# Performance work log

Measured on AMD Instinct MI355X. Metric: run time of the kernel, lower is better.

Reference implementation:

```python
import jax, jax.numpy as jnp
import numpy as np

B, T, D, H = 4, 2048, 1024, 16
Dh = D // H

def setup_inputs() -> dict:
    key = jax.random.key(0)
    ks = jax.random.split(key, 6)
    scale = 1.0 / np.sqrt(D)
    return {
        "x": jax.random.normal(ks[0], (B, T, D), dtype=jnp.float32),
        "W_q": jax.random.normal(ks[1], (D, D), dtype=jnp.float32) * scale,
        "W_k": jax.random.normal(ks[2], (D, D), dtype=jnp.float32) * scale,
        "W_v": jax.random.normal(ks[3], (D, D), dtype=jnp.float32) * scale,
        "W_o": jax.random.normal(ks[4], (D, D), dtype=jnp.float32) * scale,
        "b_o": jax.random.normal(ks[5], (D,), dtype=jnp.float32) * 0.02,
    }

def reference(x, W_q, W_k, W_v, W_o, b_o):
    # Linear weights stored torch-style (out, in): y = x @ W.T
    def split_heads(z):
        return z.reshape(B, T, H, Dh).transpose(0, 2, 1, 3)  # [B,H,T,Dh]
    q = split_heads(x @ W_q.T)
    k = split_heads(x @ W_k.T)
    v = split_heads(x @ W_v.T)
    scale = Dh ** -0.5
    attn = jnp.einsum('bhqd,bhkd->bhqk', q, k) * scale  # [B,H,T,T]
    causal = jnp.tril(jnp.ones((T, T), dtype=bool))
    attn = jnp.where(causal[None, None], attn, -jnp.inf)
    attn = jax.nn.softmax(attn, axis=-1)
    y = jnp.einsum('bhqk,bhkd->bhqd', attn, v)  # [B,H,T,Dh]
    y = y.transpose(0, 2, 1, 3).reshape(B, T, D)
    return y @ W_o.T + b_o
```

## Files before the change

kernel.cpp:

```cpp
#include <hip/hip_runtime.h>
#include <hip/hip_bf16.h>
#include <stdint.h>

#define B_   4
#define T_   2048
#define H_   16
#define MTOT (B_ * T_)
#define NQKV 3072
#define QSC  0.18033688f

typedef __attribute__((ext_vector_type(8))) __bf16 bf16x8;
typedef __attribute__((ext_vector_type(4))) float f32x4;
typedef __attribute__((ext_vector_type(16))) float f32x16;
typedef __attribute__((ext_vector_type(4))) float f4v;
typedef __attribute__((ext_vector_type(4))) unsigned short us4;
typedef __attribute__((ext_vector_type(8))) unsigned short us8;
typedef __attribute__((ext_vector_type(4))) unsigned int u32x4;

static __device__ __forceinline__ unsigned short f2bf(float f) {
  __hip_bfloat16 h = __float2bfloat16(f);
  return __builtin_bit_cast(unsigned short, h);
}

static __device__ __forceinline__ float fast_exp2(float x) {
#if __has_builtin(__builtin_amdgcn_exp2f)
  return __builtin_amdgcn_exp2f(x);
#else
  float r; asm("v_exp_f32 %0, %1" : "=v"(r) : "v"(x)); return r;
#endif
}

static __device__ __forceinline__ void async16(const void* g, void* l) {
  __builtin_amdgcn_global_load_lds(
      (const __attribute__((address_space(1))) void*)g,
      (__attribute__((address_space(3))) void*)l, 16, 0, 0);
}

__global__ __launch_bounds__(256) void cvt_all(
    const float* __restrict__ x, const float* __restrict__ Wq,
    const float* __restrict__ Wk, const float* __restrict__ Wv,
    const float* __restrict__ Wo, unsigned short* __restrict__ xb,
    unsigned short* __restrict__ wqkv, unsigned short* __restrict__ wo) {
  int i = blockIdx.x * blockDim.x + threadIdx.x;
  const float* s; unsigned short* d; int j;
  if (i < 2097152)      { s = x;  d = xb;             j = i; }
  else if (i < 2359296) { s = Wq; d = wqkv;           j = i - 2097152; }
  else if (i < 2621440) { s = Wk; d = wqkv + 1048576; j = i - 2359296; }
  else if (i < 2883584) { s = Wv; d = wqkv + 2097152; j = i - 2621440; }
  else                  { s = Wo; d = wo;             j = i - 2883584; }
  f4v v = reinterpret_cast<const f4v*>(s)[j];
  us4 o;
  o.x = f2bf(v.x); o.y = f2bf(v.y); o.z = f2bf(v.z); o.w = f2bf(v.w);
  reinterpret_cast<us4*>(d)[j] = o;
}

template <int MODE>
__global__ __launch_bounds__(256) void gemm_bt(
    const unsigned short* __restrict__ A,
    const unsigned short* __restrict__ Bw,
    unsigned short* __restrict__ Cb,
    float* __restrict__ Cf,
    const float* __restrict__ bias,
    int K, int N) {
  __shared__ __align__(16) unsigned short As[128 * 32];
  __shared__ __align__(16) unsigned short Bs[128 * 32];

  const int t = threadIdx.x;
  const int lane = t & 63;
  const int w = t >> 6;
  const int lr = lane & 15;
  const int lg = lane >> 4;
  const int wm = w >> 1;
  const int wn = w & 1;
  const int m0 = blockIdx.y * 128;
  const int n0 = blockIdx.x * 128;

  f32x4 acc[4][4];
#pragma unroll
  for (int i = 0; i < 4; ++i)
#pragma unroll
    for (int j = 0; j < 4; ++j) acc[i][j] = (f32x4){0.f, 0.f, 0.f, 0.f};

  const int srow = t >> 2;
  const int scol = (t & 3) * 8;
  const unsigned short* ga = A + (size_t)(m0 + srow) * K + scol;
  const unsigned short* gb = Bw + (size_t)(n0 + srow) * K + scol;

  for (int k0 = 0; k0 < K; k0 += 32) {
    async16(ga + k0,                  &As[t * 8]);
    async16(ga + k0 + (size_t)64 * K, &As[2048 + t * 8]);
    async16(gb + k0,                  &Bs[t * 8]);
    async16(gb + k0 + (size_t)64 * K, &Bs[2048 + t * 8]);
    __syncthreads();

    bf16x8 af[4], bfr[4];
#pragma unroll
    for (int mi = 0; mi < 4; ++mi)
      af[mi] = *(const bf16x8*)&As[(wm * 64 + mi * 16 + lr) * 32 + lg * 8];
#pragma unroll
    for (int ni = 0; ni < 4; ++ni)
      bfr[ni] = *(const bf16x8*)&Bs[(wn * 64 + ni * 16 + lr) * 32 + lg * 8];
#pragma unroll
    for (int mi = 0; mi < 4; ++mi)
#pragma unroll
      for (int ni = 0; ni < 4; ++ni)
        acc[mi][ni] = __builtin_amdgcn_mfma_f32_16x16x32_bf16(
            af[mi], bfr[ni], acc[mi][ni], 0, 0, 0);
    __syncthreads();
  }

#pragma unroll
  for (int mi = 0; mi < 4; ++mi) {
    const int row = m0 + wm * 64 + mi * 16 + lg * 4;
#pragma unroll
    for (int ni = 0; ni < 4; ++ni) {
      const int col = n0 + wn * 64 + ni * 16 + lr;
#pragma unroll
      for (int r = 0; r < 4; ++r) {
        if (MODE == 1) {
          Cf[(size_t)(row + r) * N + col] = acc[mi][ni][r] + bias[col];
        } else {
          float v = acc[mi][ni][r];
          if (col < 1024) v *= QSC;
          Cb[(size_t)(row + r) * N + col] = f2bf(v);
        }
      }
    }
  }
}

__global__ __launch_bounds__(512, 2) void attn_kernel(
    const unsigned short* __restrict__ qkv, unsigned short* __restrict__ ob) {
  const int bid = blockIdx.x;
  const int qg = (bid < 256) ? (7 - (bid >> 6)) : ((bid - 256) >> 6);
  const int pair = bid & 63;
  const int b = pair >> 4;
  const int h = pair & 15;
  const int t = threadIdx.x;
  const int w = t >> 6;
  const int lane = t & 63;
  const int l31 = lane & 31;
  const int hi = lane >> 5;

  const int q0w = qg * 256 + w * 32;
  const int myBound = qg * 4 + (w >> 1);
  const int NT2 = qg * 2 + 2;

  __shared__ __align__(16) unsigned short Ks[2][128 * 64];
  __shared__ __align__(16) unsigned short Vs[2][128 * 64];

  const size_t rowbase = (size_t)(b * T_) * NQKV;

  bf16x8 Qf[4];
  {
    const unsigned short* qp =
        qkv + rowbase + (size_t)(q0w + l31) * NQKV + h * 64 + hi * 8;
#pragma unroll
    for (int m = 0; m < 4; ++m) Qf[m] = *(const bf16x8*)(qp + m * 16);
  }

  const int krow = t >> 3;
  const int kg = (t & 7) ^ (krow & 7);
  const unsigned short* kbase =
      qkv + rowbase + 1024 + h * 64 + kg * 8 + (size_t)krow * NQKV;
  const int kvr = t >> 3;
  const int dc = t & 7;
  const unsigned short* vbase =
      qkv + rowbase + 2048 + h * 64 + dc * 8 + (size_t)kvr * NQKV;

  float m_i = -INFINITY, l_i = 0.f;
  f32x16 o[2];
#pragma unroll
  for (int r = 0; r < 16; ++r) { o[0][r] = 0.f; o[1][r] = 0.f; }

#define VSCATTER(Vb, v0, v1)                                     \
  {                                                              \
    _Pragma("unroll") for (int i = 0; i < 8; ++i) {              \
      const int sw = dc ^ i;                                     \
      const int c0 = (kvr >> 3) ^ sw;                            \
      unsigned short* vp = (Vb) + (dc * 8 + i) * 128 + (kvr & 7);\
      vp[c0 * 8] = (v0)[i];                                      \
      vp[c0 * 8 + 64] = (v1)[i];                                 \
    }                                                            \
  }

  {
    async16(kbase, &Ks[0][t * 8]);
    async16(kbase + (size_t)64 * NQKV, &Ks[0][4096 + t * 8]);
    us8 v0 = *(const us8*)vbase;
    us8 v1 = *(const us8*)(vbase + (size_t)64 * NQKV);
    VSCATTER(&Vs[0][0], v0, v1);
  }

  int cur = 0;
  for (int kt = 0; kt < NT2; ++kt) {
    __syncthreads();

    const bool pf = (kt + 1 < NT2);
    us8 v0, v1;
    if (pf) {
      const size_t off = (size_t)(kt + 1) * 128 * NQKV;
      async16(kbase + off, &Ks[cur ^ 1][t * 8]);
      async16(kbase + off + (size_t)64 * NQKV, &Ks[cur ^ 1][4096 + t * 8]);
      v0 = *(const us8*)(vbase + off);
      v1 = *(const us8*)(vbase + off + (size_t)64 * NQKV);
    }

    const unsigned short* Kb = Ks[cur];
    const unsigned short* Vb = Vs[cur];

#pragma unroll
    for (int kh = 0; kh < 2; ++kh) {
      const int kt64 = kt * 2 + kh;
      if (kt64 > myBound) break;

      f32x16 a0, a1;
#pragma unroll
      for (int r = 0; r < 16; ++r) { a0[r] = 0.f; a1[r] = 0.f; }
      {
        const int rb0 = (kh * 64 + l31) * 64;
        const int rb1 = (kh * 64 + 32 + l31) * 64;
        const int r7 = l31 & 7;
        __builtin_amdgcn_s_setprio(1);
#pragma unroll
        for (int m = 0; m < 4; ++m) {
          const int c = (((m << 1) | hi) ^ r7) * 8;
          bf16x8 kf0 = *(const bf16x8*)&Kb[rb0 + c];
          bf16x8 kf1 = *(const bf16x8*)&Kb[rb1 + c];
          a0 = __builtin_amdgcn_mfma_f32_32x32x16_bf16(kf0, Qf[m], a0, 0, 0, 0);
          a1 = __builtin_amdgcn_mfma_f32_32x32x16_bf16(kf1, Qf[m], a1, 0, 0, 0);
        }
        __builtin_amdgcn_s_setprio(0);
      }

      if (kt64 == myBound) {
        const int qglob = q0w + l31;
#pragma unroll
        for (int r = 0; r < 16; ++r) {
          const int kvb = kt64 * 64 + (r & 3) + ((r >> 2) << 3) + (hi << 2);
          if (kvb > qglob) a0[r] = -INFINITY;
          if (kvb + 32 > qglob) a1[r] = -INFINITY;
        }
      }

      float m8[8];
#pragma unroll
      for (int j = 0; j < 8; ++j)
        m8[j] = fmaxf(fmaxf(a0[j], a0[j + 8]), fmaxf(a1[j], a1[j + 8]));
      float pmax = fmaxf(fmaxf(fmaxf(m8[0], m8[4]), fmaxf(m8[1], m8[5])),
                         fmaxf(fmaxf(m8[2], m8[6]), fmaxf(m8[3], m8[7])));
      pmax = fmaxf(pmax, __shfl_xor(pmax, 32));
      if (__any(pmax > m_i + 8.f)) {
        const float mnew = fmaxf(m_i, pmax);
        const float al = fast_exp2(m_i - mnew);
        m_i = mnew;
        l_i *= al;
#pragma unroll
        for (int r = 0; r < 16; ++r) { o[0][r] *= al; o[1][r] *= al; }
      }

#pragma unroll
      for (int r = 0; r < 16; ++r) {
        a0[r] = fast_exp2(a0[r] - m_i);
        a1[r] = fast_exp2(a1[r] - m_i);
      }
      float s8[8];
#pragma unroll
      for (int j = 0; j < 8; ++j)
        s8[j] = (a0[j] + a0[j + 8]) + (a1[j] + a1[j + 8]);
      float rs = ((s8[0] + s8[1]) + (s8[2] + s8[3])) +
                 ((s8[4] + s8[5]) + (s8[6] + s8[7]));
      rs += __shfl_xor(rs, 32);
      l_i += rs;

      bf16x8 Pf[4];
#pragma unroll
      for (int m = 0; m < 4; ++m) {
        const int rb2 = (m & 1) * 8;
        uint32_t u0, u1, u2, u3;
        const f32x16& s = (m >> 1) ? a1 : a0;
        asm("v_cvt_pk_bf16_f32 %0, %1, %2" : "=v"(u0) : "v"(s[rb2 + 0]), "v"(s[rb2 + 1]));
        asm("v_cvt_pk_bf16_f32 %0, %1, %2" : "=v"(u1) : "v"(s[rb2 + 2]), "v"(s[rb2 + 3]));
        asm("v_cvt_pk_bf16_f32 %0, %1, %2" : "=v"(u2) : "v"(s[rb2 + 4]), "v"(s[rb2 + 5]));
        asm("v_cvt_pk_bf16_f32 %0, %1, %2" : "=v"(u3) : "v"(s[rb2 + 6]), "v"(s[rb2 + 7]));
        asm("v_permlane32_swap_b32 %0, %1" : "+v"(u0), "+v"(u2));
        asm("v_permlane32_swap_b32 %0, %1" : "+v"(u1), "+v"(u3));
        u32x4 pw = {u0, u1, u2, u3};
        Pf[m] = __builtin_bit_cast(bf16x8, pw);
      }

      __builtin_amdgcn_s_setprio(1);
#pragma unroll
      for (int dt = 0; dt < 2; ++dt) {
        const int d = dt * 32 + l31;
        const int base = d * 128 + kh * 64;
        const int dsw = ((d >> 3) ^ d) & 7;
#pragma unroll
        for (int m = 0; m < 4; ++m) {
          bf16x8 vf = *(const bf16x8*)&Vb[base + ((((m << 1) | hi) ^ dsw) & 7) * 8];
          o[dt] = __builtin_amdgcn_mfma_f32_32x32x16_bf16(vf, Pf[m], o[dt], 0, 0, 0);
        }
      }
      __builtin_amdgcn_s_setprio(0);
    }

    if (pf) VSCATTER(&Vs[cur ^ 1][0], v0, v1);
    cur ^= 1;
  }

  const float rl = 1.0f / l_i;
#pragma unroll
  for (int dt = 0; dt < 2; ++dt) {
    float s[16];
#pragma unroll
    for (int r = 0; r < 16; ++r) s[r] = o[dt][r] * rl;
    uint32_t u[8];
#pragma unroll
    for (int p = 0; p < 8; ++p)
      asm("v_cvt_pk_bf16_f32 %0, %1, %2" : "=v"(u[p]) : "v"(s[2 * p]), "v"(s[2 * p + 1]));
    asm("v_permlane32_swap_b32 %0, %1" : "+v"(u[0]), "+v"(u[2]));
    asm("v_permlane32_swap_b32 %0, %1" : "+v"(u[1]), "+v"(u[3]));
    asm("v_permlane32_swap_b32 %0, %1" : "+v"(u[4]), "+v"(u[6]));
    asm("v_permlane32_swap_b32 %0, %1" : "+v"(u[5]), "+v"(u[7]));
    unsigned short* op =
        ob + (size_t)(b * T_ + q0w + l31) * 1024 + h * 64 + dt * 32 + hi * 8;
    u32x4 c0 = {u[0], u[1], u[2], u[3]};
    u32x4 c1 = {u[4], u[5], u[6], u[7]};
    *(u32x4*)op = c0;
    *(u32x4*)(op + 16) = c1;
  }
}

extern "C" void kernel_launch(void* const* d_in, const int* in_sizes, int n_in,
                              void* d_out, int out_size, void* d_ws,
                              size_t ws_size, hipStream_t stream) {
  const float* x = (const float*)d_in[0];
  const float* Wq = (const float*)d_in[1];
  const float* Wk = (const float*)d_in[2];
  const float* Wv = (const float*)d_in[3];
  const float* Wo = (const float*)d_in[4];
  const float* bo = (const float*)d_in[5];
  float* out = (float*)d_out;

  char* ws = (char*)d_ws;
  unsigned short* xb   = (unsigned short*)(ws + 0);
  unsigned short* wqkv = (unsigned short*)(ws + 16777216);
  unsigned short* wo   = (unsigned short*)(ws + 23068672);
  unsigned short* qkv  = (unsigned short*)(ws + 25165824);
  unsigned short* ob   = (unsigned short*)(ws + 75497472);
  if (ws_size < 92274688u) return;

  cvt_all<<<12288, 256, 0, stream>>>(x, Wq, Wk, Wv, Wo, xb, wqkv, wo);

  gemm_bt<0><<<dim3(NQKV / 128, MTOT / 128), 256, 0, stream>>>(
      xb, wqkv, qkv, nullptr, nullptr, 1024, NQKV);

  attn_kernel<<<dim3(512), 512, 0, stream>>>(qkv, ob);

  gemm_bt<1><<<dim3(1024 / 128, MTOT / 128), 256, 0, stream>>>(
      ob, wo, nullptr, out, bo, 1024, 1024);
}
```

Baseline: 190.1 us.

## Shrink attention blocks to 128 queries with 64-key tiles and permlane reductions

Restructures the attention kernel from 512-thread blocks over 256 queries with 128-key tiles to 256-thread blocks over 128 queries with 64-key tiles. The grid doubles to 1024 blocks, scheduled heaviest-first in four rounds, and the V scatter and LDS layout are reworked for the smaller tile. Cross-half max and sum reductions now use v_permlane32_swap instead of shfl_xor. The goal is better load balance over the causal triangle, more resident blocks and cheaper reductions, at the cost of more K/V reloads per query and more barriers per key.

```diff
diff --git a/kernel.cpp b/kernel.cpp
--- a/kernel.cpp
+++ b/kernel.cpp
@@ -35,6 +35,15 @@
       (const __attribute__((address_space(1))) void*)g,
       (__attribute__((address_space(3))) void*)l, 16, 0, 0);
 }
+
+#define XHALF(res, x, OP)                                  \
+  {                                                        \
+    float t1_ = (x), t2_ = (x);                            \
+    asm("" : "+v"(t2_));                                   \
+    asm("v_permlane32_swap_b32 %0, %1" : "+v"(t1_), "+v"(t2_)); \
+    res = OP(t1_, t2_);                                    \
+  }
+static __device__ __forceinline__ float fadd_(float a, float b) { return a + b; }
 
 __global__ __launch_bounds__(256) void cvt_all(
     const float* __restrict__ x, const float* __restrict__ Wq,
@@ -129,11 +138,15 @@
   }
 }
 
-__global__ __launch_bounds__(512, 2) void attn_kernel(
+__global__ __launch_bounds__(256, 4) void attn_kernel(
     const unsigned short* __restrict__ qkv, unsigned short* __restrict__ ob) {
   const int bid = blockIdx.x;
-  const int qg = (bid < 256) ? (7 - (bid >> 6)) : ((bid - 256) >> 6);
   const int pair = bid & 63;
+  const int g = bid >> 6;
+  const int rnd = g >> 2, idx = g & 3;
+  const int qg = (rnd == 0) ? (15 - idx)
+               : (rnd == 1) ? (8 + idx)
+               : (rnd == 2) ? (7 - idx) : idx;
   const int b = pair >> 4;
   const int h = pair & 15;
   const int t = threadIdx.x;
@@ -142,12 +155,12 @@
   const int l31 = lane & 31;
   const int hi = lane >> 5;
 
-  const int q0w = qg * 256 + w * 32;
-  const int myBound = qg * 4 + (w >> 1);
-  const int NT2 = qg * 2 + 2;
-
-  __shared__ __align__(16) unsigned short Ks[2][128 * 64];
-  __shared__ __align__(16) unsigned short Vs[2][128 * 64];
+  const int q0w = qg * 128 + w * 32;
+  const int myBound = 2 * qg + (w >> 1);
+  const int NT = 2 * qg + 2;
+
+  __shared__ __align__(16) unsigned short Ks[2][64 * 64];
+  __shared__ __align__(16) unsigned short Vs[2][64 * 64];
 
   const size_t rowbase = (size_t)(b * T_) * NQKV;
 
@@ -159,67 +172,62 @@
     for (int m = 0; m < 4; ++m) Qf[m] = *(const bf16x8*)(qp + m * 16);
   }
 
-  const int krow = t >> 3;
-  const int kg = (t & 7) ^ (krow & 7);
+  const int kr = t >> 3;
+  const int ks = t & 7;
   const unsigned short* kbase =
-      qkv + rowbase + 1024 + h * 64 + kg * 8 + (size_t)krow * NQKV;
-  const int kvr = t >> 3;
-  const int dc = t & 7;
+      qkv + rowbase + 1024 + h * 64 + (ks ^ (kr & 7)) * 8 + (size_t)kr * NQKV;
+  const int kvr = t >> 2;
+  const int dc2 = (t & 3) * 2;
   const unsigned short* vbase =
-      qkv + rowbase + 2048 + h * 64 + dc * 8 + (size_t)kvr * NQKV;
+      qkv + rowbase + 2048 + h * 64 + dc2 * 8 + (size_t)kvr * NQKV;
 
   float m_i = -INFINITY, l_i = 0.f;
   f32x16 o[2];
 #pragma unroll
   for (int r = 0; r < 16; ++r) { o[0][r] = 0.f; o[1][r] = 0.f; }
 
-#define VSCATTER(Vb, v0, v1)                                     \
-  {                                                              \
-    _Pragma("unroll") for (int i = 0; i < 8; ++i) {              \
-      const int sw = dc ^ i;                                     \
-      const int c0 = (kvr >> 3) ^ sw;                            \
-      unsigned short* vp = (Vb) + (dc * 8 + i) * 128 + (kvr & 7);\
-      vp[c0 * 8] = (v0)[i];                                      \
-      vp[c0 * 8 + 64] = (v1)[i];                                 \
-    }                                                            \
+#define VSCATTER(Vb, v0, v1)                                       \
+  {                                                                \
+    _Pragma("unroll") for (int i = 0; i < 8; ++i) {                \
+      const int s0 = ((kvr >> 3) ^ dc2 ^ i) & 7;                   \
+      const int s1 = ((kvr >> 3) ^ (dc2 + 1) ^ i) & 7;             \
+      (Vb)[(dc2 * 8 + i) * 64 + s0 * 8 + (kvr & 7)] = (v0)[i];     \
+      (Vb)[((dc2 + 1) * 8 + i) * 64 + s1 * 8 + (kvr & 7)] = (v1)[i]; \
+    }                                                              \
   }
 
   {
     async16(kbase, &Ks[0][t * 8]);
-    async16(kbase + (size_t)64 * NQKV, &Ks[0][4096 + t * 8]);
+    async16(kbase + (size_t)32 * NQKV, &Ks[0][2048 + t * 8]);
     us8 v0 = *(const us8*)vbase;
-    us8 v1 = *(const us8*)(vbase + (size_t)64 * NQKV);
+    us8 v1 = *(const us8*)(vbase + 8);
     VSCATTER(&Vs[0][0], v0, v1);
   }
 
   int cur = 0;
-  for (int kt = 0; kt < NT2; ++kt) {
+  for (int kt = 0; kt < NT; ++kt) {
     __syncthreads();
 
-    const bool pf = (kt + 1 < NT2);
+    const bool pf = (kt + 1 < NT);
     us8 v0, v1;
     if (pf) {
-      const size_t off = (size_t)(kt + 1) * 128 * NQKV;
+      const size_t off = (size_t)(kt + 1) * 64 * NQKV;
       async16(kbase + off, &Ks[cur ^ 1][t * 8]);
-      async16(kbase + off + (size_t)64 * NQKV, &Ks[cur ^ 1][4096 + t * 8]);
+      async16(kbase + off + (size_t)32 * NQKV, &Ks[cur ^ 1][2048 + t * 8]);
       v0 = *(const us8*)(vbase + off);
-      v1 = *(const us8*)(vbase + off + (size_t)64 * NQKV);
+      v1 = *(const us8*)(vbase + off + 8);
     }
 
-    const unsigned short* Kb = Ks[cur];
-    const unsigned short* Vb = Vs[cur];
-
-#pragma unroll
-    for (int kh = 0; kh < 2; ++kh) {
-      const int kt64 = kt * 2 + kh;
-      if (kt64 > myBound) break;
+    if (kt <= myBound) {
+      const unsigned short* Kb = Ks[cur];
+      const unsigned short* Vb = Vs[cur];
 
       f32x16 a0, a1;
 #pragma unroll
       for (int r = 0; r < 16; ++r) { a0[r] = 0.f; a1[r] = 0.f; }
       {
-        const int rb0 = (kh * 64 + l31) * 64;
-        const int rb1 = (kh * 64 + 32 + l31) * 64;
+        const int rb0 = l31 * 64;
+        const int rb1 = (32 + l31) * 64;
         const int r7 = l31 & 7;
         __builtin_amdgcn_s_setprio(1);
 #pragma unroll
@@ -233,11 +241,11 @@
         __builtin_amdgcn_s_setprio(0);
       }
 
-      if (kt64 == myBound) {
+      if (kt == myBound) {
         const int qglob = q0w + l31;
 #pragma unroll
         for (int r = 0; r < 16; ++r) {
-          const int kvb = kt64 * 64 + (r & 3) + ((r >> 2) << 3) + (hi << 2);
+          const int kvb = kt * 64 + (r & 3) + ((r >> 2) << 3) + (hi << 2);
           if (kvb > qglob) a0[r] = -INFINITY;
           if (kvb + 32 > qglob) a1[r] = -INFINITY;
         }
@@ -247,9 +255,10 @@
 #pragma unroll
       for (int j = 0; j < 8; ++j)
         m8[j] = fmaxf(fmaxf(a0[j], a0[j + 8]), fmaxf(a1[j], a1[j + 8]));
-      float pmax = fmaxf(fmaxf(fmaxf(m8[0], m8[4]), fmaxf(m8[1], m8[5])),
-                         fmaxf(fmaxf(m8[2], m8[6]), fmaxf(m8[3], m8[7])));
-      pmax = fmaxf(pmax, __shfl_xor(pmax, 32));
+      float pp = fmaxf(fmaxf(fmaxf(m8[0], m8[4]), fmaxf(m8[1], m8[5])),
+                       fmaxf(fmaxf(m8[2], m8[6]), fmaxf(m8[3], m8[7])));
+      float pmax;
+      XHALF(pmax, pp, fmaxf);
       if (__any(pmax > m_i + 8.f)) {
         const float mnew = fmaxf(m_i, pmax);
         const float al = fast_exp2(m_i - mnew);
@@ -268,9 +277,10 @@
 #pragma unroll
       for (int j = 0; j < 8; ++j)
         s8[j] = (a0[j] + a0[j + 8]) + (a1[j] + a1[j + 8]);
-      float rs = ((s8[0] + s8[1]) + (s8[2] + s8[3])) +
+      float rp = ((s8[0] + s8[1]) + (s8[2] + s8[3])) +
                  ((s8[4] + s8[5]) + (s8[6] + s8[7]));
-      rs += __shfl_xor(rs, 32);
+      float rs;
+      XHALF(rs, rp, fadd_);
       l_i += rs;
 
       bf16x8 Pf[4];
@@ -293,7 +303,7 @@
 #pragma unroll
       for (int dt = 0; dt < 2; ++dt) {
         const int d = dt * 32 + l31;
-        const int base = d * 128 + kh * 64;
+        const int base = d * 64;
         const int dsw = ((d >> 3) ^ d) & 7;
 #pragma unroll
         for (int m = 0; m < 4; ++m) {
@@ -355,7 +365,7 @@
   gemm_bt<0><<<dim3(NQKV / 128, MTOT / 128), 256, 0, stream>>>(
       xb, wqkv, qkv, nullptr, nullptr, 1024, NQKV);
 
-  attn_kernel<<<dim3(512), 512, 0, stream>>>(qkv, ob);
+  attn_kernel<<<dim3(1024), 256, 0, stream>>>(qkv, ob);
 
   gemm_bt<1><<<dim3(1024 / 128, MTOT / 128), 256, 0, stream>>>(
       ob, wo, nullptr, out, bo, 1024, 1024);
```

Measured after the change: 184.4 us. 3.0% less time.
